# Kernel optimization log

Hardware: AMD Instinct MI355X
Metric: run time of the kernel (lower is better)

The kernel has to match this reference:

```python
import jax, jax.numpy as jnp
import numpy as np

D_MODEL = 1024
N_HEADS = 8
HEAD_DIM = D_MODEL // N_HEADS
B, T = 4, 2048


def setup_inputs() -> dict:
    key = jax.random.key(0)
    ks = jax.random.split(key, 10)
    x = jax.random.normal(ks[0], (B, T, D_MODEL), dtype=jnp.float32)
    # causal mask: True entries are masked (matches torch masked_fill semantics)
    mask = jnp.triu(jnp.ones((T, T), dtype=bool), k=1)

    def xavier(k, shape):
        fan_in, fan_out = shape[1], shape[0]
        lim = float(np.sqrt(6.0 / (fan_in + fan_out)))
        return jax.random.uniform(k, shape, jnp.float32, -lim, lim)

    Wq = xavier(ks[1], (D_MODEL, D_MODEL)); bq = jnp.zeros((D_MODEL,), jnp.float32)
    Wk = xavier(ks[2], (D_MODEL, D_MODEL)); bk = jnp.zeros((D_MODEL,), jnp.float32)
    Wv = xavier(ks[3], (D_MODEL, D_MODEL)); bv = jnp.zeros((D_MODEL,), jnp.float32)
    Wo = xavier(ks[4], (D_MODEL, D_MODEL)); bo = jnp.zeros((D_MODEL,), jnp.float32)
    return {"x": x, "mask": mask, "Wq": Wq, "bq": bq, "Wk": Wk, "bk": bk,
            "Wv": Wv, "bv": bv, "Wo": Wo, "bo": bo}


def reference(x, mask, Wq, bq, Wk, bk, Wv, bv, Wo, bo):
    Bsz, Tlen, _ = x.shape
    # torch Linear: y = x @ W.T + b
    Q = (x @ Wq.T + bq).reshape(Bsz, Tlen, N_HEADS, HEAD_DIM).transpose(0, 2, 1, 3)  # [B,H,T,Dh]
    K = (x @ Wk.T + bk).reshape(Bsz, Tlen, N_HEADS, HEAD_DIM).transpose(0, 2, 1, 3)  # [B,H,T,Dh]
    V_shared = x @ Wv.T + bv  # [B,T,D] shared across heads
    scale = 1.0 / jnp.sqrt(jnp.float32(HEAD_DIM))
    scores = jnp.einsum('bhqd,bhkd->bhqk', Q, K) * scale  # [B,H,T,T]
    scores = jnp.where(mask[None, None, :, :], jnp.float32(-1e9), scores)
    attn_per_head = jax.nn.softmax(scores, axis=-1)
    alpha_agg = attn_per_head.mean(axis=1)  # [B,T,T] head-averaged attention
    out = jnp.einsum('bqk,bkd->bqd', alpha_agg, V_shared) @ Wo.T + bo
    return out, alpha_agg
```

## Files before the change

kernel.cpp:

```cpp
#include <hip/hip_runtime.h>
#include <hip/hip_bf16.h>

#define D_MODEL 1024
#define NH 8
#define HD 128
#define BATCH 4
#define TSEQ 2048
#define MROWS (BATCH * TSEQ)
#define QKV_LD 3072
#define SBAND 131072
#define SBATCH ((size_t)SBAND * 136)

typedef __attribute__((ext_vector_type(8))) __bf16 bf16x8;
typedef __attribute__((ext_vector_type(4))) __bf16 bf16x4;
typedef __attribute__((ext_vector_type(4))) float f32x4;
typedef __attribute__((ext_vector_type(8))) unsigned short u16x8;

#define SC2 0.1275174441680632f

__device__ __forceinline__ void gload16(const void* g, void* lds) {
  __builtin_amdgcn_global_load_lds(
      (const __attribute__((address_space(1))) unsigned int*)g,
      (__attribute__((address_space(3))) unsigned int*)lds, 16, 0, 0);
}

__device__ __forceinline__ dim3 swz_grid() {
  const int nx = gridDim.x, ny = gridDim.y;
  const int nwg = nx * ny * gridDim.z;
  int L = blockIdx.x + nx * (blockIdx.y + ny * blockIdx.z);
  const int q = nwg >> 3, r = nwg & 7;
  const int xcd = L & 7, idx = L >> 3;
  int t = (xcd < r ? xcd * (q + 1) : r * (q + 1) + (xcd - r) * q) + idx;
  dim3 o;
  o.x = t % nx; t /= nx;
  o.y = t % ny;
  o.z = t / ny;
  return o;
}

__global__ __launch_bounds__(256) void cvt_f32_to_bf16(const float* __restrict__ in,
                                                       __bf16* __restrict__ out, int n4) {
  int i = blockIdx.x * 256 + threadIdx.x;
  if (i < n4) {
    float4 v = reinterpret_cast<const float4*>(in)[i];
    bf16x4 o;
    o[0] = (__bf16)v.x; o[1] = (__bf16)v.y; o[2] = (__bf16)v.z; o[3] = (__bf16)v.w;
    reinterpret_cast<bf16x4*>(out)[i] = o;
  }
}

__global__ __launch_bounds__(256) void cvt4_weights(const float* __restrict__ w0,
                                                    const float* __restrict__ w1,
                                                    const float* __restrict__ w2,
                                                    const float* __restrict__ w3,
                                                    __bf16* __restrict__ out) {
  const int per = D_MODEL * D_MODEL / 4;
  int i = blockIdx.x * 256 + threadIdx.x;
  int m = i / per, j = i - m * per;
  const float* src = (m == 0) ? w0 : (m == 1) ? w1 : (m == 2) ? w2 : w3;
  float4 v = reinterpret_cast<const float4*>(src)[j];
  bf16x4 o;
  o[0] = (__bf16)v.x; o[1] = (__bf16)v.y; o[2] = (__bf16)v.z; o[3] = (__bf16)v.w;
  reinterpret_cast<bf16x4*>(out)[i] = o;
}

__global__ __launch_bounds__(256) void concat_bias(const float* __restrict__ a,
                                                   const float* __restrict__ b,
                                                   const float* __restrict__ c,
                                                   float* __restrict__ o) {
  int i = blockIdx.x * 256 + threadIdx.x;
  if (i < 3072) o[i] = (i < 1024) ? a[i] : (i < 2048) ? b[i - 1024] : c[i - 2048];
}

template <bool BF16OUT, bool CAUSAL, bool AFP32>
__global__ __launch_bounds__(256) void gemm128(const void* __restrict__ Aip,
                                               const __bf16* __restrict__ Bp,
                                               const float* __restrict__ bias,
                                               void* __restrict__ Yp, int K, int ldy,
                                               size_t sA, size_t sB, size_t sY) {
  __shared__ __bf16 As[2][128 * 32];
  __shared__ __bf16 Bs[2][128 * 32];
  const dim3 bi = swz_grid();
  const int tid = threadIdx.x;
  const int w = tid >> 6, l = tid & 63;
  const int lr = l & 15, lg = l >> 4;
  const int m0 = bi.y * 128, n0 = bi.x * 128;
  const int z = bi.z;
  const __bf16* Ab = AFP32 ? nullptr : (const __bf16*)Aip + z * sA;
  const float* Af = AFP32 ? (const float*)Aip + z * sA : nullptr;
  const __bf16* Bb = Bp + z * sB;
  const int wm = w >> 1, wn = w & 1;
  f32x4 acc[4][4] = {};
  const int Klim = CAUSAL ? (m0 + 128 < K ? m0 + 128 : K) : K;
  const int nt = Klim >> 5;

  auto stage = [&](int t, int buf) {
    const int k0 = t << 5;
    if constexpr (!AFP32) {
#pragma unroll
      for (int i = 0; i < 2; ++i) {
        int s = w * 128 + i * 64 + l;
        int row = s >> 2, scp = s & 3;
        int sc = scp ^ ((row >> 1) & 3);
        gload16(Ab + (size_t)(m0 + row) * K + k0 + sc * 8, (char*)As[buf] + s * 16);
      }
    } else {
#pragma unroll
      for (int i = 0; i < 2; ++i) {
        int s = w * 128 + i * 64 + l;
        int row = s >> 2, sc = s & 3;
        const float* src = Af + (size_t)(m0 + row) * K + k0 + sc * 8;
        float4 lo = *reinterpret_cast<const float4*>(src);
        float4 hi = *reinterpret_cast<const float4*>(src + 4);
        bf16x8 v;
        v[0] = (__bf16)lo.x; v[1] = (__bf16)lo.y; v[2] = (__bf16)lo.z; v[3] = (__bf16)lo.w;
        v[4] = (__bf16)hi.x; v[5] = (__bf16)hi.y; v[6] = (__bf16)hi.z; v[7] = (__bf16)hi.w;
        int p = row * 4 + (sc ^ ((row >> 1) & 3));
        *reinterpret_cast<bf16x8*>((char*)As[buf] + p * 16) = v;
      }
    }
#pragma unroll
    for (int i = 0; i < 2; ++i) {
      int s = w * 128 + i * 64 + l;
      int row = s >> 2, scp = s & 3;
      int sc = scp ^ ((row >> 1) & 3);
      gload16(Bb + (size_t)(n0 + row) * K + k0 + sc * 8, (char*)Bs[buf] + s * 16);
    }
  };

  stage(0, 0);
  __syncthreads();
  int cur = 0;
  for (int t = 0; t < nt; ++t) {
    if (t + 1 < nt) stage(t + 1, cur ^ 1);
    bf16x8 af[4], bf[4];
#pragma unroll
    for (int f = 0; f < 4; ++f) {
      int ar = wm * 64 + f * 16 + lr;
      af[f] = *reinterpret_cast<const bf16x8*>((const char*)As[cur] + ar * 64 +
                                               ((lg ^ ((ar >> 1) & 3)) * 16));
      int br = wn * 64 + f * 16 + lr;
      bf[f] = *reinterpret_cast<const bf16x8*>((const char*)Bs[cur] + br * 64 +
                                               ((lg ^ ((br >> 1) & 3)) * 16));
    }
#pragma unroll
    for (int mf = 0; mf < 4; ++mf)
#pragma unroll
      for (int nf = 0; nf < 4; ++nf)
        acc[mf][nf] = __builtin_amdgcn_mfma_f32_16x16x32_bf16(af[mf], bf[nf], acc[mf][nf], 0, 0, 0);
    __syncthreads();
    cur ^= 1;
  }

#pragma unroll
  for (int mf = 0; mf < 4; ++mf) {
#pragma unroll
    for (int nf = 0; nf < 4; ++nf) {
#pragma unroll
      for (int r = 0; r < 4; ++r) {
        int grow = m0 + wm * 64 + mf * 16 + lg * 4 + r;
        int gcol = n0 + wn * 64 + nf * 16 + lr;
        float v = acc[mf][nf][r];
        if (bias) v += bias[gcol];
        if constexpr (BF16OUT)
          ((__bf16*)Yp + z * sY)[(size_t)grow * ldy + gcol] = (__bf16)v;
        else
          ((float*)Yp + z * sY)[(size_t)grow * ldy + gcol] = v;
      }
    }
  }
}

__global__ __launch_bounds__(256) void transpose_v(const __bf16* __restrict__ V,
                                                   __bf16* __restrict__ Vt) {
  __shared__ unsigned short tile[64 * 72];
  const int b = blockIdx.z;
  const int t0 = blockIdx.x * 64, d0 = blockIdx.y * 64;
  const int tid = threadIdx.x;
#pragma unroll
  for (int i = 0; i < 2; ++i) {
    int s = i * 256 + tid;
    int r = s >> 3, c8 = s & 7;
    u16x8 v = *reinterpret_cast<const u16x8*>(V + ((size_t)b * TSEQ + t0 + r) * QKV_LD + d0 + c8 * 8);
    *reinterpret_cast<u16x8*>(&tile[r * 72 + c8 * 8]) = v;
  }
  __syncthreads();
#pragma unroll
  for (int i = 0; i < 2; ++i) {
    int s = i * 256 + tid;
    int dr = s >> 3, t8 = s & 7;
    u16x8 o;
#pragma unroll
    for (int j = 0; j < 8; ++j) o[j] = tile[(t8 * 8 + j) * 72 + dr];
    *reinterpret_cast<u16x8*>(Vt + ((size_t)b * D_MODEL + d0 + dr) * TSEQ + t0 + t8 * 8) = o;
  }
}

__global__ __launch_bounds__(256) void score_gemm(const __bf16* __restrict__ QKV,
                                                  __bf16* __restrict__ S,
                                                  float* __restrict__ lsum,
                                                  int b0, size_t sstride) {
  __shared__ __bf16 As[2][128 * 32];
  __shared__ __bf16 Bs[2][128 * 32];
  const dim3 bi = swz_grid();
  const int tid = threadIdx.x;
  const int w = tid >> 6, l = tid & 63;
  const int lr = l & 15, lg = l >> 4;
  const int wm = w >> 1, wn = w & 1;
  const int idx = bi.x;
  const int h = bi.y;
  const int zz = bi.z;
  const int b = b0 + zz;
  int qt = (int)((sqrtf(8.f * (float)idx + 1.f) - 1.f) * 0.5f);
  while ((qt + 1) * (qt + 2) / 2 <= idx) ++qt;
  while (qt * (qt + 1) / 2 > idx) --qt;
  const int kt = idx - qt * (qt + 1) / 2;
  const int q0 = qt * 128, k0 = kt * 128;
  const int kext = (qt + 1) * 128;
  const bool diag = (kt == qt);

  const __bf16* Ab = QKV + (size_t)(b * TSEQ + q0) * QKV_LD + h * HD;
  const __bf16* Bb = QKV + (size_t)(b * TSEQ + k0) * QKV_LD + 1024 + h * HD;

  auto stage = [&](int t, int buf) {
#pragma unroll
    for (int i = 0; i < 2; ++i) {
      int s = w * 128 + i * 64 + l;
      int row = s >> 2, scp = s & 3;
      int sc = scp ^ ((row >> 1) & 3);
      gload16(Ab + (size_t)row * QKV_LD + t * 32 + sc * 8, (char*)As[buf] + s * 16);
    }
#pragma unroll
    for (int i = 0; i < 2; ++i) {
      int s = w * 128 + i * 64 + l;
      int row = s >> 2, scp = s & 3;
      int sc = scp ^ ((row >> 1) & 3);
      gload16(Bb + (size_t)row * QKV_LD + t * 32 + sc * 8, (char*)Bs[buf] + s * 16);
    }
  };

  f32x4 acc[4][4] = {};
  stage(0, 0);
  __syncthreads();
  int cur = 0;
#pragma unroll
  for (int t = 0; t < 4; ++t) {
    if (t < 3) stage(t + 1, cur ^ 1);
    bf16x8 af[4], bf[4];
#pragma unroll
    for (int f = 0; f < 4; ++f) {
      int ar = wm * 64 + f * 16 + lr;
      af[f] = *reinterpret_cast<const bf16x8*>((const char*)As[cur] + ar * 64 +
                                               ((lg ^ ((ar >> 1) & 3)) * 16));
      int br = wn * 64 + f * 16 + lr;
      bf[f] = *reinterpret_cast<const bf16x8*>((const char*)Bs[cur] + br * 64 +
                                               ((lg ^ ((br >> 1) & 3)) * 16));
    }
#pragma unroll
    for (int mf = 0; mf < 4; ++mf)
#pragma unroll
      for (int nf = 0; nf < 4; ++nf)
        acc[mf][nf] = __builtin_amdgcn_mfma_f32_16x16x32_bf16(af[mf], bf[nf], acc[mf][nf], 0, 0, 0);
    __syncthreads();
    cur ^= 1;
  }

  __bf16* Sb = S + zz * sstride + (size_t)SBAND * ((qt * (qt + 1)) >> 1) +
               (size_t)h * 128 * kext + k0;
  float ls[4][4] = {};
#pragma unroll
  for (int mf = 0; mf < 4; ++mf) {
#pragma unroll
    for (int r = 0; r < 4; ++r) {
      int row = wm * 64 + mf * 16 + lg * 4 + r;
      __bf16* srow = Sb + (size_t)row * kext;
#pragma unroll
      for (int nf = 0; nf < 4; ++nf) {
        int col = wn * 64 + nf * 16 + lr;
        float v = acc[mf][nf][r];
        srow[col] = (__bf16)v;
        if (!diag || col <= row) ls[mf][r] += exp2f(v * SC2);
      }
    }
  }
#pragma unroll
  for (int m = 1; m < 16; m <<= 1)
#pragma unroll
    for (int mf = 0; mf < 4; ++mf)
#pragma unroll
      for (int r = 0; r < 4; ++r) ls[mf][r] += __shfl_xor(ls[mf][r], m, 64);
  if (lr == 0) {
#pragma unroll
    for (int mf = 0; mf < 4; ++mf)
#pragma unroll
      for (int r = 0; r < 4; ++r)
        atomicAdd(&lsum[((size_t)(b * NH + h)) * TSEQ + q0 + wm * 64 + mf * 16 + lg * 4 + r],
                  ls[mf][r]);
  }
}

__global__ __launch_bounds__(256) void alpha_stream(const __bf16* __restrict__ S,
                                                    const float* __restrict__ lsum,
                                                    float* __restrict__ alpha,
                                                    int b0, size_t sstride) {
  const int q = blockIdx.x;
  const int zz = blockIdx.y;
  const int b = b0 + zz;
  const int qt = q >> 7;
  const int kext = (qt + 1) * 128;
  const int k0 = threadIdx.x * 8;
  float* arow = alpha + ((size_t)(b * TSEQ + q)) * TSEQ + k0;
  if (k0 >= kext) {
    float4 zzf = {0.f, 0.f, 0.f, 0.f};
    *reinterpret_cast<float4*>(arow) = zzf;
    *reinterpret_cast<float4*>(arow + 4) = zzf;
    return;
  }
  const __bf16* Sb = S + zz * sstride + (size_t)SBAND * ((qt * (qt + 1)) >> 1) +
                     (size_t)(q & 127) * kext + k0;
  const size_t hstride = (size_t)128 * kext;
  float o[8] = {};
#pragma unroll
  for (int h = 0; h < NH; ++h) {
    float li = 1.0f / (8.0f * lsum[((size_t)(b * NH + h)) * TSEQ + q]);
    bf16x8 s8 = *reinterpret_cast<const bf16x8*>(Sb + h * hstride);
#pragma unroll
    for (int j = 0; j < 8; ++j) o[j] += exp2f((float)s8[j] * SC2) * li;
  }
#pragma unroll
  for (int j = 0; j < 8; ++j)
    if (k0 + j > q) o[j] = 0.f;
  float4 lo = {o[0], o[1], o[2], o[3]};
  float4 hi = {o[4], o[5], o[6], o[7]};
  *reinterpret_cast<float4*>(arow) = lo;
  *reinterpret_cast<float4*>(arow + 4) = hi;
}

extern "C" void kernel_launch(void* const* d_in, const int* in_sizes, int n_in,
                              void* d_out, int out_size, void* d_ws, size_t ws_size,
                              hipStream_t stream) {
  const float* x  = (const float*)d_in[0];
  const float* Wq = (const float*)d_in[2];
  const float* bq = (const float*)d_in[3];
  const float* Wk = (const float*)d_in[4];
  const float* bk = (const float*)d_in[5];
  const float* Wv = (const float*)d_in[6];
  const float* bv = (const float*)d_in[7];
  const float* Wo = (const float*)d_in[8];
  const float* bo = (const float*)d_in[9];

  float* out_f = (float*)d_out;
  float* alpha = out_f + (size_t)MROWS * D_MODEL;

  char* p = (char*)d_ws;
  __bf16* xb   = (__bf16*)p; p += (size_t)MROWS * D_MODEL * 2;
  __bf16* wqb  = (__bf16*)p; p += (size_t)D_MODEL * D_MODEL * 2;
  __bf16* wkb  = (__bf16*)p; p += (size_t)D_MODEL * D_MODEL * 2;
  __bf16* wvb  = (__bf16*)p; p += (size_t)D_MODEL * D_MODEL * 2;
  __bf16* wob  = (__bf16*)p; p += (size_t)D_MODEL * D_MODEL * 2;
  __bf16* qkv  = (__bf16*)p; p += (size_t)MROWS * QKV_LD * 2;
  __bf16* vtb  = (__bf16*)p; p += (size_t)BATCH * D_MODEL * TSEQ * 2;
  float* lsum  = (float*)p;  p += (size_t)BATCH * NH * TSEQ * 4;
  float* bcat  = (float*)p;  p += 3072 * 4;
  __bf16* sbuf = (__bf16*)p;
  __bf16* midb = xb;

  size_t used = (size_t)((char*)sbuf - (char*)d_ws);
  size_t sb1 = SBATCH * 2;
  int NB = 1;
  if (ws_size >= used + 4 * sb1) NB = 4;
  else if (ws_size >= used + 2 * sb1) NB = 2;
  size_t sstride = (NB > 1) ? SBATCH : 0;

  hipMemsetAsync(lsum, 0, (size_t)BATCH * NH * TSEQ * 4, stream);

  {
    int n4 = MROWS * D_MODEL / 4;
    cvt_f32_to_bf16<<<n4 / 256, 256, 0, stream>>>(x, xb, n4);
    int w4 = 4 * D_MODEL * D_MODEL / 4;
    cvt4_weights<<<w4 / 256, 256, 0, stream>>>(Wq, Wk, Wv, Wo, wqb);
    concat_bias<<<12, 256, 0, stream>>>(bq, bk, bv, bcat);
  }

  gemm128<true, false, false><<<dim3(QKV_LD / 128, MROWS / 128), 256, 0, stream>>>(
      xb, wqb, bcat, qkv, D_MODEL, QKV_LD, 0, 0, 0);

  transpose_v<<<dim3(TSEQ / 64, D_MODEL / 64, BATCH), 256, 0, stream>>>(qkv + 2048, vtb);

  for (int b0 = 0; b0 < BATCH; b0 += NB) {
    score_gemm<<<dim3(136, NH, NB), 256, 0, stream>>>(qkv, sbuf, lsum, b0, sstride);
    alpha_stream<<<dim3(TSEQ, NB), 256, 0, stream>>>(sbuf, lsum, alpha, b0, sstride);
  }

  gemm128<true, true, true><<<dim3(D_MODEL / 128, TSEQ / 128, BATCH), 256, 0, stream>>>(
      alpha, vtb, nullptr, midb, TSEQ, D_MODEL,
      (size_t)TSEQ * TSEQ, (size_t)D_MODEL * TSEQ, (size_t)TSEQ * D_MODEL);

  gemm128<false, false, false><<<dim3(D_MODEL / 128, MROWS / 128), 256, 0, stream>>>(
      midb, wob, bo, out_f, D_MODEL, D_MODEL, 0, 0, 0);
}
```

Measured before the change: 363.3 us.

## Stage GEMM epilogues through LDS for coalesced stores and store exp'd scores

The bf16-output GEMM and the score GEMM now write their accumulator tiles into a shared-memory buffer (reusing the operand staging space) with an XOR swizzle, then issue coalesced 16-byte global stores instead of scattered 2-byte stores. The score kernel also stores exp2 of the scaled scores rather than the raw scores, so the alpha kernel no longer recomputes the exponential per element. This adds an extra barrier and LDS round-trip per tile. Storing exponentials in bf16 also changes precision characteristics compared with storing raw scores.

```diff
diff --git a/kernel.cpp b/kernel.cpp
--- a/kernel.cpp
+++ b/kernel.cpp
@@ -78,8 +78,9 @@
                                                const float* __restrict__ bias,
                                                void* __restrict__ Yp, int K, int ldy,
                                                size_t sA, size_t sB, size_t sY) {
-  __shared__ __bf16 As[2][128 * 32];
-  __shared__ __bf16 Bs[2][128 * 32];
+  __shared__ __bf16 sm[16384];
+  __bf16* const As0 = sm;
+  __bf16* const Bs0 = sm + 8192;
   const dim3 bi = swz_grid();
   const int tid = threadIdx.x;
   const int w = tid >> 6, l = tid & 63;
@@ -96,13 +97,15 @@
 
   auto stage = [&](int t, int buf) {
     const int k0 = t << 5;
+    __bf16* As = As0 + buf * 4096;
+    __bf16* Bs = Bs0 + buf * 4096;
     if constexpr (!AFP32) {
 #pragma unroll
       for (int i = 0; i < 2; ++i) {
         int s = w * 128 + i * 64 + l;
         int row = s >> 2, scp = s & 3;
         int sc = scp ^ ((row >> 1) & 3);
-        gload16(Ab + (size_t)(m0 + row) * K + k0 + sc * 8, (char*)As[buf] + s * 16);
+        gload16(Ab + (size_t)(m0 + row) * K + k0 + sc * 8, (char*)As + s * 16);
       }
     } else {
 #pragma unroll
@@ -116,7 +119,7 @@
         v[0] = (__bf16)lo.x; v[1] = (__bf16)lo.y; v[2] = (__bf16)lo.z; v[3] = (__bf16)lo.w;
         v[4] = (__bf16)hi.x; v[5] = (__bf16)hi.y; v[6] = (__bf16)hi.z; v[7] = (__bf16)hi.w;
         int p = row * 4 + (sc ^ ((row >> 1) & 3));
-        *reinterpret_cast<bf16x8*>((char*)As[buf] + p * 16) = v;
+        *reinterpret_cast<bf16x8*>((char*)As + p * 16) = v;
       }
     }
 #pragma unroll
@@ -124,7 +127,7 @@
       int s = w * 128 + i * 64 + l;
       int row = s >> 2, scp = s & 3;
       int sc = scp ^ ((row >> 1) & 3);
-      gload16(Bb + (size_t)(n0 + row) * K + k0 + sc * 8, (char*)Bs[buf] + s * 16);
+      gload16(Bb + (size_t)(n0 + row) * K + k0 + sc * 8, (char*)Bs + s * 16);
     }
   };
 
@@ -137,10 +140,10 @@
 #pragma unroll
     for (int f = 0; f < 4; ++f) {
       int ar = wm * 64 + f * 16 + lr;
-      af[f] = *reinterpret_cast<const bf16x8*>((const char*)As[cur] + ar * 64 +
+      af[f] = *reinterpret_cast<const bf16x8*>((const char*)(As0 + cur * 4096) + ar * 64 +
                                                ((lg ^ ((ar >> 1) & 3)) * 16));
       int br = wn * 64 + f * 16 + lr;
-      bf[f] = *reinterpret_cast<const bf16x8*>((const char*)Bs[cur] + br * 64 +
+      bf[f] = *reinterpret_cast<const bf16x8*>((const char*)(Bs0 + cur * 4096) + br * 64 +
                                                ((lg ^ ((br >> 1) & 3)) * 16));
     }
 #pragma unroll
@@ -152,22 +155,45 @@
     cur ^= 1;
   }
 
-#pragma unroll
-  for (int mf = 0; mf < 4; ++mf) {
-#pragma unroll
-    for (int nf = 0; nf < 4; ++nf) {
+  if constexpr (BF16OUT) {
+    float bv[4];
+#pragma unroll
+    for (int nf = 0; nf < 4; ++nf) bv[nf] = bias ? bias[n0 + wn * 64 + nf * 16 + lr] : 0.f;
+#pragma unroll
+    for (int mf = 0; mf < 4; ++mf)
 #pragma unroll
       for (int r = 0; r < 4; ++r) {
-        int grow = m0 + wm * 64 + mf * 16 + lg * 4 + r;
-        int gcol = n0 + wn * 64 + nf * 16 + lr;
-        float v = acc[mf][nf][r];
-        if (bias) v += bias[gcol];
-        if constexpr (BF16OUT)
-          ((__bf16*)Yp + z * sY)[(size_t)grow * ldy + gcol] = (__bf16)v;
-        else
+        int row = wm * 64 + mf * 16 + lg * 4 + r;
+#pragma unroll
+        for (int nf = 0; nf < 4; ++nf) {
+          int col = wn * 64 + nf * 16 + lr;
+          int pseg = (col >> 3) ^ (row & 15);
+          sm[row * 128 + pseg * 8 + (col & 7)] = (__bf16)(acc[mf][nf][r] + bv[nf]);
+        }
+      }
+    __syncthreads();
+    __bf16* Yb = (__bf16*)Yp + z * sY;
+#pragma unroll
+    for (int i = 0; i < 8; ++i) {
+      int s = i * 256 + tid;
+      int row = s >> 4, pseg = s & 15;
+      int lseg = pseg ^ (row & 15);
+      bf16x8 v = *reinterpret_cast<bf16x8*>(sm + row * 128 + pseg * 8);
+      *reinterpret_cast<bf16x8*>(&Yb[(size_t)(m0 + row) * ldy + n0 + lseg * 8]) = v;
+    }
+  } else {
+#pragma unroll
+    for (int mf = 0; mf < 4; ++mf)
+#pragma unroll
+      for (int nf = 0; nf < 4; ++nf)
+#pragma unroll
+        for (int r = 0; r < 4; ++r) {
+          int grow = m0 + wm * 64 + mf * 16 + lg * 4 + r;
+          int gcol = n0 + wn * 64 + nf * 16 + lr;
+          float v = acc[mf][nf][r];
+          if (bias) v += bias[gcol];
           ((float*)Yp + z * sY)[(size_t)grow * ldy + gcol] = v;
-      }
-    }
+        }
   }
 }
 
@@ -200,8 +226,9 @@
                                                   __bf16* __restrict__ S,
                                                   float* __restrict__ lsum,
                                                   int b0, size_t sstride) {
-  __shared__ __bf16 As[2][128 * 32];
-  __shared__ __bf16 Bs[2][128 * 32];
+  __shared__ __bf16 sm[16384];
+  __bf16* const As0 = sm;
+  __bf16* const Bs0 = sm + 8192;
   const dim3 bi = swz_grid();
   const int tid = threadIdx.x;
   const int w = tid >> 6, l = tid & 63;
@@ -223,19 +250,21 @@
   const __bf16* Bb = QKV + (size_t)(b * TSEQ + k0) * QKV_LD + 1024 + h * HD;
 
   auto stage = [&](int t, int buf) {
+    __bf16* As = As0 + buf * 4096;
+    __bf16* Bs = Bs0 + buf * 4096;
 #pragma unroll
     for (int i = 0; i < 2; ++i) {
       int s = w * 128 + i * 64 + l;
       int row = s >> 2, scp = s & 3;
       int sc = scp ^ ((row >> 1) & 3);
-      gload16(Ab + (size_t)row * QKV_LD + t * 32 + sc * 8, (char*)As[buf] + s * 16);
+      gload16(Ab + (size_t)row * QKV_LD + t * 32 + sc * 8, (char*)As + s * 16);
     }
 #pragma unroll
     for (int i = 0; i < 2; ++i) {
       int s = w * 128 + i * 64 + l;
       int row = s >> 2, scp = s & 3;
       int sc = scp ^ ((row >> 1) & 3);
-      gload16(Bb + (size_t)row * QKV_LD + t * 32 + sc * 8, (char*)Bs[buf] + s * 16);
+      gload16(Bb + (size_t)row * QKV_LD + t * 32 + sc * 8, (char*)Bs + s * 16);
     }
   };
 
@@ -250,10 +279,10 @@
 #pragma unroll
     for (int f = 0; f < 4; ++f) {
       int ar = wm * 64 + f * 16 + lr;
-      af[f] = *reinterpret_cast<const bf16x8*>((const char*)As[cur] + ar * 64 +
+      af[f] = *reinterpret_cast<const bf16x8*>((const char*)(As0 + cur * 4096) + ar * 64 +
                                                ((lg ^ ((ar >> 1) & 3)) * 16));
       int br = wn * 64 + f * 16 + lr;
-      bf[f] = *reinterpret_cast<const bf16x8*>((const char*)Bs[cur] + br * 64 +
+      bf[f] = *reinterpret_cast<const bf16x8*>((const char*)(Bs0 + cur * 4096) + br * 64 +
                                                ((lg ^ ((br >> 1) & 3)) * 16));
     }
 #pragma unroll
@@ -265,24 +294,21 @@
     cur ^= 1;
   }
 
-  __bf16* Sb = S + zz * sstride + (size_t)SBAND * ((qt * (qt + 1)) >> 1) +
-               (size_t)h * 128 * kext + k0;
   float ls[4][4] = {};
 #pragma unroll
-  for (int mf = 0; mf < 4; ++mf) {
+  for (int mf = 0; mf < 4; ++mf)
 #pragma unroll
     for (int r = 0; r < 4; ++r) {
       int row = wm * 64 + mf * 16 + lg * 4 + r;
-      __bf16* srow = Sb + (size_t)row * kext;
 #pragma unroll
       for (int nf = 0; nf < 4; ++nf) {
         int col = wn * 64 + nf * 16 + lr;
-        float v = acc[mf][nf][r];
-        srow[col] = (__bf16)v;
-        if (!diag || col <= row) ls[mf][r] += exp2f(v * SC2);
+        float ev = exp2f(acc[mf][nf][r] * SC2);
+        int pseg = (col >> 3) ^ (row & 15);
+        sm[row * 128 + pseg * 8 + (col & 7)] = (__bf16)ev;
+        if (!diag || col <= row) ls[mf][r] += ev;
       }
     }
-  }
 #pragma unroll
   for (int m = 1; m < 16; m <<= 1)
 #pragma unroll
@@ -296,6 +322,17 @@
       for (int r = 0; r < 4; ++r)
         atomicAdd(&lsum[((size_t)(b * NH + h)) * TSEQ + q0 + wm * 64 + mf * 16 + lg * 4 + r],
                   ls[mf][r]);
+  }
+  __syncthreads();
+  __bf16* Sb = S + zz * sstride + (size_t)SBAND * ((qt * (qt + 1)) >> 1) +
+               (size_t)h * 128 * kext + k0;
+#pragma unroll
+  for (int i = 0; i < 8; ++i) {
+    int s = i * 256 + tid;
+    int row = s >> 4, pseg = s & 15;
+    int lseg = pseg ^ (row & 15);
+    bf16x8 v = *reinterpret_cast<bf16x8*>(sm + row * 128 + pseg * 8);
+    *reinterpret_cast<bf16x8*>(&Sb[(size_t)row * kext + lseg * 8]) = v;
   }
 }
 
@@ -325,7 +362,7 @@
     float li = 1.0f / (8.0f * lsum[((size_t)(b * NH + h)) * TSEQ + q]);
     bf16x8 s8 = *reinterpret_cast<const bf16x8*>(Sb + h * hstride);
 #pragma unroll
-    for (int j = 0; j < 8; ++j) o[j] += exp2f((float)s8[j] * SC2) * li;
+    for (int j = 0; j < 8; ++j) o[j] += (float)s8[j] * li;
   }
 #pragma unroll
   for (int j = 0; j < 8; ++j)
```

Result: no change. 360.6 us (-0.8%).
